# Kernel tuning notes

Measured on AMD Instinct MI355X. Metric: run time of the kernel, lower is better.

## Reference

```python
import jax, jax.numpy as jnp
import numpy as np

C, H, P = 128, 4, 8  # d_model, n_heads, n_points (n_levels=1)
D = C // H


def setup_inputs() -> dict:
    key = jax.random.key(0)
    ks = jax.random.split(key, 14)
    B, Y, X = 2, 200, 200
    N = Y * X
    s = 0.05
    inp = {
        "query": jax.random.normal(ks[0], (B, N, C), jnp.float32),
        "query_pos": jax.random.normal(ks[1], (B, N, C), jnp.float32),
        # MSDeformAttn params
        "Wv": jax.random.normal(ks[2], (C, C), jnp.float32) * s,
        "bv": jnp.zeros((C,), jnp.float32),
        "Woff": jax.random.normal(ks[3], (C, H * P * 2), jnp.float32) * s,
        "boff": jax.random.normal(ks[4], (H * P * 2,), jnp.float32) * s,
        "Wattn": jax.random.normal(ks[5], (C, H * P), jnp.float32) * s,
        "battn": jnp.zeros((H * P,), jnp.float32),
        "Wout1": jax.random.normal(ks[6], (C, C), jnp.float32) * s,  # MSDeformAttn.output_proj
        "bout1": jnp.zeros((C,), jnp.float32),
        "Wout2": jax.random.normal(ks[7], (C, C), jnp.float32) * s,  # wrapper output_proj
        "bout2": jnp.zeros((C,), jnp.float32),
        "Y": Y,
        "X": X,
    }
    return inp


def _deform_attn(q, v_in, Wv, bv, Woff, boff, Wattn, battn, Wout1, bout1, Y, X):
    B, N, _ = q.shape
    # reference points: grid centers, stacked (y, x) normalized (as in source)
    ref_y = (jnp.arange(Y, dtype=jnp.float32) + 0.5) / Y
    ref_x = (jnp.arange(X, dtype=jnp.float32) + 0.5) / X
    ry, rx = jnp.meshgrid(ref_y, ref_x, indexing="ij")
    ref = jnp.stack([ry.reshape(-1), rx.reshape(-1)], -1)  # (N, 2)

    value = (v_in @ Wv + bv).reshape(B, Y, X, H, D).transpose(0, 3, 1, 2, 4)  # (B,H,Y,X,D)
    off = (q @ Woff + boff).reshape(B, N, H, P, 2)
    attn = jax.nn.softmax((q @ Wattn + battn).reshape(B, N, H, P), axis=-1)

    # offset normalizer = (W, H) = (X, Y); loc = ref + off/norm  (faithful to source)
    norm = jnp.array([X, Y], jnp.float32)
    loc = ref[None, :, None, None, :] + off / norm  # (B,N,H,P,2)

    # grid_sample bilinear, align_corners=False, zero padding; channel 0 = x, 1 = y
    gx = loc[..., 0] * X - 0.5
    gy = loc[..., 1] * Y - 0.5
    x0 = jnp.floor(gx)
    y0 = jnp.floor(gy)
    wx1 = gx - x0
    wy1 = gy - y0
    x0i = x0.astype(jnp.int32)
    y0i = y0.astype(jnp.int32)

    b_idx = jnp.arange(B)[:, None, None, None]
    h_idx = jnp.arange(H)[None, None, :, None]

    def gather(yi, xi, w):
        valid = (yi >= 0) & (yi < Y) & (xi >= 0) & (xi < X)
        yc = jnp.clip(yi, 0, Y - 1)
        xc = jnp.clip(xi, 0, X - 1)
        v = value[b_idx, h_idx, yc, xc]  # (B,N,H,P,D)
        return v * (w * valid)[..., None]

    sampled = (
        gather(y0i, x0i, (1 - wy1) * (1 - wx1))
        + gather(y0i, x0i + 1, (1 - wy1) * wx1)
        + gather(y0i + 1, x0i, wy1 * (1 - wx1))
        + gather(y0i + 1, x0i + 1, wy1 * wx1)
    )
    out = (sampled * attn[..., None]).sum(axis=3).reshape(B, N, C)
    return out @ Wout1 + bout1


def reference(query, query_pos, Wv, bv, Woff, boff, Wattn, battn, Wout1, bout1, Wout2, bout2, Y, X):
    residual = query
    q = query + query_pos
    out = _deform_attn(q, q, Wv, bv, Woff, boff, Wattn, battn, Wout1, bout1, Y, X)
    out = out @ Wout2 + bout2  # wrapper output_proj; dropout in eval mode = identity
    return out + residual
```

## Files before the change

kernel.cpp:

```cpp
#include <hip/hip_runtime.h>
#include <hip/hip_bf16.h>

#define BQ 2
#define YY 200
#define XX 200
#define NQ 40000
#define CC 128
#define MTOT 80000
#define NCOL 224
#define NTILES 5000

typedef __attribute__((ext_vector_type(8))) short short8;
typedef __attribute__((ext_vector_type(4))) short short4v;
typedef __attribute__((ext_vector_type(4))) float f32x4;

static __device__ __forceinline__ unsigned short f2bf(float f) {
    union { float f; unsigned int u; } v; v.f = f;
    unsigned int r = v.u + 0x7FFF + ((v.u >> 16) & 1);
    return (unsigned short)(r >> 16);
}
static __device__ __forceinline__ unsigned short f2bf_hw(float f) {
    __hip_bfloat16 h = __float2bfloat16(f);
    unsigned short s;
    __builtin_memcpy(&s, &h, 2);
    return s;
}

__global__ void prep_wcat(const float* __restrict__ Wv, const float* __restrict__ Woff,
                          const float* __restrict__ Wattn, unsigned short* __restrict__ WcatT) {
    int idx = blockIdx.x * 256 + threadIdx.x;
    if (idx >= NCOL * CC) return;
    int c = idx >> 7, k = idx & 127;
    float w = (c < 128) ? Wv[k * 128 + c]
            : (c < 192) ? Woff[k * 64 + (c - 128)]
                        : Wattn[k * 32 + (c - 192)];
    WcatT[c * 128 + k] = f2bf(w);
}

__global__ void prep_w12(const float* __restrict__ Wout1, const float* __restrict__ Wout2,
                         const float* __restrict__ bout1, const float* __restrict__ bout2,
                         unsigned short* __restrict__ W12T, float* __restrict__ b12) {
    int idx = blockIdx.x * 256 + threadIdx.x;
    int c = idx >> 7, k = idx & 127;
    float s = 0.f;
    for (int j = 0; j < 128; ++j) s += Wout1[k * 128 + j] * Wout2[j * 128 + c];
    W12T[c * 128 + k] = f2bf(s);
    if (k == 0) {
        float t = bout2[c];
        for (int j = 0; j < 128; ++j) t += bout1[j] * Wout2[j * 128 + c];
        b12[c] = t;
    }
}

__global__ __launch_bounds__(256) void qsum_kernel(const float* __restrict__ query,
                                                   const float* __restrict__ qpos,
                                                   unsigned short* __restrict__ qbf) {
    const size_t total = (size_t)MTOT * CC / 8;
    for (size_t c = (size_t)blockIdx.x * 256 + threadIdx.x; c < total;
         c += (size_t)gridDim.x * 256) {
        const float4* a = (const float4*)(query + c * 8);
        const float4* b = (const float4*)(qpos + c * 8);
        float4 a0 = a[0], a1 = a[1], b0 = b[0], b1 = b[1];
        short8 w;
        w[0] = (short)f2bf_hw(a0.x + b0.x); w[1] = (short)f2bf_hw(a0.y + b0.y);
        w[2] = (short)f2bf_hw(a0.z + b0.z); w[3] = (short)f2bf_hw(a0.w + b0.w);
        w[4] = (short)f2bf_hw(a1.x + b1.x); w[5] = (short)f2bf_hw(a1.y + b1.y);
        w[6] = (short)f2bf_hw(a1.z + b1.z); w[7] = (short)f2bf_hw(a1.w + b1.w);
        *(short8*)(qbf + c * 8) = w;
    }
}

__global__ __launch_bounds__(256, 2) void g1_kernel(
    const unsigned short* __restrict__ qbf, const unsigned short* __restrict__ WcatT,
    const float* __restrict__ bv, const float* __restrict__ boff, const float* __restrict__ battn,
    unsigned short* __restrict__ value_bf, float* __restrict__ off_out, float* __restrict__ logits_out)
{
    const int tid = threadIdx.x;
    const int group = blockIdx.x & 3;
    const int gblk = blockIdx.x >> 2;
    const int lane = tid & 63;
    const int arow = lane & 15, kq = lane >> 4;
    const int wid = gblk * 4 + (tid >> 6);
    const int tg0 = group * 4;
    const int NT = (group == 3) ? 2 : 4;

    short8 bf[4][4];
#pragma unroll
    for (int t = 0; t < 4; ++t) {
        if (t < NT) {
#pragma unroll
            for (int ks = 0; ks < 4; ++ks)
                bf[t][ks] = *(const short8*)(WcatT + (size_t)((tg0 + t) * 16 + arow) * 128 + ks * 32 + kq * 8);
        }
    }

    f32x4 biasv[4];
#pragma unroll
    for (int t = 0; t < 4; ++t) {
        if (t < NT) {
            const float* bp = (group < 2) ? (bv + (tg0 + t) * 16 + kq * 4)
                            : (group == 2) ? (boff + (tg0 + t - 8) * 16 + kq * 4)
                                           : (battn + (tg0 + t - 12) * 16 + kq * 4);
            float4 b4 = *(const float4*)bp;
            biasv[t] = (f32x4){b4.x, b4.y, b4.z, b4.w};
        }
    }

    for (int tile = wid; tile < NTILES; tile += 1024) {
        const char* pa = (const char*)qbf + (size_t)(tile * 16 + arow) * 256 + kq * 16;
        short8 af[4];
#pragma unroll
        for (int ks = 0; ks < 4; ++ks) af[ks] = *(const short8*)(pa + ks * 64);

        f32x4 acc[4];
#pragma unroll
        for (int t = 0; t < 4; ++t) acc[t] = biasv[t];

#pragma unroll
        for (int ks = 0; ks < 4; ++ks) {
#pragma unroll
            for (int t = 0; t < 4; ++t) {
                if (t < NT)
                    acc[t] = __builtin_amdgcn_mfma_f32_16x16x32_bf16(bf[t][ks], af[ks], acc[t], 0, 0, 0);
            }
        }

        const int row = tile * 16 + arow;
        if (group < 2) {
#pragma unroll
            for (int t = 0; t < 4; ++t) {
                short4v pv;
                pv[0] = (short)f2bf_hw(acc[t][0]); pv[1] = (short)f2bf_hw(acc[t][1]);
                pv[2] = (short)f2bf_hw(acc[t][2]); pv[3] = (short)f2bf_hw(acc[t][3]);
                *(short4v*)(value_bf + (size_t)row * 128 + (tg0 + t) * 16 + kq * 4) = pv;
            }
        } else if (group == 2) {
#pragma unroll
            for (int t = 0; t < 4; ++t) {
                float4 o = make_float4(acc[t][0], acc[t][1], acc[t][2], acc[t][3]);
                *(float4*)(off_out + (size_t)row * 64 + (tg0 + t - 8) * 16 + kq * 4) = o;
            }
        } else {
#pragma unroll
            for (int t = 0; t < 2; ++t) {
                float4 o = make_float4(acc[t][0], acc[t][1], acc[t][2], acc[t][3]);
                *(float4*)(logits_out + (size_t)row * 32 + (tg0 + t - 12) * 16 + kq * 4) = o;
            }
        }
    }
}

__global__ __launch_bounds__(256) void sample_kernel(
    const unsigned short* __restrict__ value_bf, const float* __restrict__ off_in,
    const float* __restrict__ logits, unsigned short* __restrict__ sampled)
{
    __shared__ int S[8][32][8];

    const int tid = threadIdx.x;
    const int qi = tid >> 5;
    const int lane = tid & 31;
    const int r = blockIdx.x * 8 + qi;
    const int b = (r >= NQ) ? 1 : 0;
    const int n = r - b * NQ;
    const int yq = n / XX, xq = n - yq * XX;

    {
        float lg = logits[(size_t)r * 32 + lane];
        float m = lg;
        m = fmaxf(m, __shfl_xor(m, 1));
        m = fmaxf(m, __shfl_xor(m, 2));
        m = fmaxf(m, __shfl_xor(m, 4));
        float e = __expf(lg - m);
        float s = e;
        s += __shfl_xor(s, 1);
        s += __shfl_xor(s, 2);
        s += __shfl_xor(s, 4);
        float aw = e / s;

        float2 o = ((const float2*)(off_in + (size_t)r * 64))[lane];
        float gx = (float)yq + o.x;
        float gy = (float)xq + o.y;
        float fx = floorf(gx), fy = floorf(gy);
        int x0 = (int)fx, y0 = (int)fy;
        float wx1 = gx - fx, wy1 = gy - fy;
        float vx0 = ((unsigned)x0 < XX) ? 1.f : 0.f;
        float vx1 = ((unsigned)(x0 + 1) < XX) ? 1.f : 0.f;
        float vy0 = ((unsigned)y0 < YY) ? 1.f : 0.f;
        float vy1 = ((unsigned)(y0 + 1) < YY) ? 1.f : 0.f;
        int x0c = min(max(x0, 0), XX - 1);
        int x1c = min(max(x0 + 1, 0), XX - 1);
        int y0c = min(max(y0, 0), YY - 1);
        int y1c = min(max(y0 + 1, 0), YY - 1);
        int hb = (lane >> 3) * 64;
        int rowA = y0c * XX, rowB = y1c * XX;
        int4 addrs;
        addrs.x = (rowA + x0c) * 256 + hb;
        addrs.y = (rowA + x1c) * 256 + hb;
        addrs.z = (rowB + x0c) * 256 + hb;
        addrs.w = (rowB + x1c) * 256 + hb;
        int4 wts;
        wts.x = __float_as_int((1.f - wx1) * vx0);
        wts.y = __float_as_int(wx1 * vx1);
        wts.z = __float_as_int(aw * (1.f - wy1) * vy0);
        wts.w = __float_as_int(aw * wy1 * vy1);
        *(int4*)&S[qi][lane][0] = addrs;
        *(int4*)&S[qi][lane][4] = wts;
    }
    __syncthreads();

    const char* vb = (const char*)(value_bf + (size_t)b * NQ * 128);
    const int cb = (lane & 15) * 4;
    const int g16 = lane >> 4;

    float2 acc[2];
    acc[0] = make_float2(0.f, 0.f);
    acc[1] = make_float2(0.f, 0.f);

#pragma unroll
    for (int i = 0; i < 16; ++i) {
        const int hp = g16 * 16 + i;
        int4 ai = *(const int4*)&S[qi][hp][0];
        int4 wi = *(const int4*)&S[qi][hp][4];
        float wxa = __int_as_float(wi.x);
        float wxb = __int_as_float(wi.y);
        float wya = __int_as_float(wi.z);
        float wyb = __int_as_float(wi.w);

        unsigned int u00 = *(const unsigned int*)(vb + ai.x + cb);
        unsigned int u01 = *(const unsigned int*)(vb + ai.y + cb);
        unsigned int u10 = *(const unsigned int*)(vb + ai.z + cb);
        unsigned int u11 = *(const unsigned int*)(vb + ai.w + cb);

        float f00l = __uint_as_float(u00 << 16), f00h = __uint_as_float(u00 & 0xFFFF0000u);
        float f01l = __uint_as_float(u01 << 16), f01h = __uint_as_float(u01 & 0xFFFF0000u);
        float f10l = __uint_as_float(u10 << 16), f10h = __uint_as_float(u10 & 0xFFFF0000u);
        float f11l = __uint_as_float(u11 << 16), f11h = __uint_as_float(u11 & 0xFFFF0000u);

        float tal = fmaf(wxa, f00l, wxb * f01l);
        float tbl = fmaf(wxa, f10l, wxb * f11l);
        float tah = fmaf(wxa, f00h, wxb * f01h);
        float tbh = fmaf(wxa, f10h, wxb * f11h);

        const int j = i >> 3;
        acc[j].x = fmaf(wya, tal, acc[j].x);
        acc[j].x = fmaf(wyb, tbl, acc[j].x);
        acc[j].y = fmaf(wya, tah, acc[j].y);
        acc[j].y = fmaf(wyb, tbh, acc[j].y);
    }

    char* sp = (char*)(sampled + (size_t)r * 128);
#pragma unroll
    for (int j = 0; j < 2; ++j) {
        unsigned int packed = ((unsigned int)f2bf(acc[j].y) << 16) | (unsigned int)f2bf(acc[j].x);
        *(unsigned int*)(sp + (g16 * 2 + j) * 64 + cb) = packed;
    }
}

__global__ __launch_bounds__(256, 2) void g2_kernel(
    const unsigned short* __restrict__ sampled, const unsigned short* __restrict__ W12T,
    const float* __restrict__ b12, const float* __restrict__ query, float* __restrict__ out)
{
    const int tid = threadIdx.x;
    const int group = blockIdx.x & 1;
    const int gblk = blockIdx.x >> 1;
    const int lane = tid & 63;
    const int arow = lane & 15, kq = lane >> 4;
    const int wid = gblk * 4 + (tid >> 6);
    const int tg0 = group * 4;

    short8 bf[4][4];
#pragma unroll
    for (int t = 0; t < 4; ++t)
#pragma unroll
        for (int ks = 0; ks < 4; ++ks)
            bf[t][ks] = *(const short8*)(W12T + (size_t)((tg0 + t) * 16 + arow) * 128 + ks * 32 + kq * 8);

    f32x4 biasv[4];
#pragma unroll
    for (int t = 0; t < 4; ++t) {
        float4 b4 = *(const float4*)(b12 + (tg0 + t) * 16 + kq * 4);
        biasv[t] = (f32x4){b4.x, b4.y, b4.z, b4.w};
    }

    for (int tile = wid; tile < NTILES; tile += 2048) {
        const char* pa = (const char*)sampled + (size_t)(tile * 16 + arow) * 256 + kq * 16;
        short8 af[4];
#pragma unroll
        for (int ks = 0; ks < 4; ++ks) af[ks] = *(const short8*)(pa + ks * 64);

        f32x4 acc[4];
#pragma unroll
        for (int t = 0; t < 4; ++t) acc[t] = biasv[t];

#pragma unroll
        for (int ks = 0; ks < 4; ++ks)
#pragma unroll
            for (int t = 0; t < 4; ++t)
                acc[t] = __builtin_amdgcn_mfma_f32_16x16x32_bf16(bf[t][ks], af[ks], acc[t], 0, 0, 0);

        const int row = tile * 16 + arow;
#pragma unroll
        for (int t = 0; t < 4; ++t) {
            size_t idx = (size_t)row * 128 + (tg0 + t) * 16 + kq * 4;
            float4 q4 = *(const float4*)(query + idx);
            float4 o = make_float4(acc[t][0] + q4.x, acc[t][1] + q4.y,
                                   acc[t][2] + q4.z, acc[t][3] + q4.w);
            *(float4*)(out + idx) = o;
        }
    }
}

extern "C" void kernel_launch(void* const* d_in, const int* in_sizes, int n_in,
                              void* d_out, int out_size, void* d_ws, size_t ws_size,
                              hipStream_t stream) {
    const float* query = (const float*)d_in[0];
    const float* qpos  = (const float*)d_in[1];
    const float* Wv    = (const float*)d_in[2];
    const float* bv    = (const float*)d_in[3];
    const float* Woff  = (const float*)d_in[4];
    const float* boff  = (const float*)d_in[5];
    const float* Wattn = (const float*)d_in[6];
    const float* battn = (const float*)d_in[7];
    const float* Wout1 = (const float*)d_in[8];
    const float* bout1 = (const float*)d_in[9];
    const float* Wout2 = (const float*)d_in[10];
    const float* bout2 = (const float*)d_in[11];
    float* out = (float*)d_out;

    char* ws = (char*)d_ws;
    unsigned short* value_bf = (unsigned short*)(ws);
    float*          off_buf  = (float*)(ws + 20480000);
    float*          logits   = (float*)(ws + 40960000);
    unsigned short* sampled  = (unsigned short*)(ws + 51200000);
    unsigned short* WcatT    = (unsigned short*)(ws + 71680000);
    unsigned short* W12T     = (unsigned short*)(ws + 71680000 + 57344);
    float*          b12      = (float*)(ws + 71680000 + 57344 + 32768);

    unsigned short* qbf = sampled;

    prep_wcat<<<112, 256, 0, stream>>>(Wv, Woff, Wattn, WcatT);
    prep_w12<<<64, 256, 0, stream>>>(Wout1, Wout2, bout1, bout2, W12T, b12);
    qsum_kernel<<<2048, 256, 0, stream>>>(query, qpos, qbf);
    g1_kernel<<<1024, 256, 0, stream>>>(qbf, WcatT, bv, boff, battn,
                                        value_bf, off_buf, logits);
    sample_kernel<<<MTOT / 8, 256, 0, stream>>>(value_bf, off_buf, logits, sampled);
    g2_kernel<<<1024, 256, 0, stream>>>(sampled, W12T, b12, query, out);
}
```

Baseline: 126.2 us.

## Remap GEMM block indices, pad sample LDS tables, and use packed FMA

The GEMM kernels now map block index to column group with high bits and row block with low bits, so consecutive blocks share the same weight tile instead of interleaving groups. The sampling kernel splits its shared address/weight table into padded int4 arrays with an interleaved slot layout to cut LDS bank conflicts. It also rewrites the bilinear accumulation with 2-wide float vectors so the compiler can emit packed FMA, using split accumulators summed at the end. The remap assumes fixed grid sizes (256 and 512 row blocks per group) that must match the launch configuration.

```diff
diff --git a/kernel.cpp b/kernel.cpp
--- a/kernel.cpp
+++ b/kernel.cpp
@@ -13,6 +13,7 @@
 typedef __attribute__((ext_vector_type(8))) short short8;
 typedef __attribute__((ext_vector_type(4))) short short4v;
 typedef __attribute__((ext_vector_type(4))) float f32x4;
+typedef __attribute__((ext_vector_type(2))) float f32x2;
 
 static __device__ __forceinline__ unsigned short f2bf(float f) {
     union { float f; unsigned int u; } v; v.f = f;
@@ -76,8 +77,8 @@
     unsigned short* __restrict__ value_bf, float* __restrict__ off_out, float* __restrict__ logits_out)
 {
     const int tid = threadIdx.x;
-    const int group = blockIdx.x & 3;
-    const int gblk = blockIdx.x >> 2;
+    const int group = blockIdx.x >> 8;
+    const int gblk = blockIdx.x & 255;
     const int lane = tid & 63;
     const int arow = lane & 15, kq = lane >> 4;
     const int wid = gblk * 4 + (tid >> 6);
@@ -154,7 +155,8 @@
     const unsigned short* __restrict__ value_bf, const float* __restrict__ off_in,
     const float* __restrict__ logits, unsigned short* __restrict__ sampled)
 {
-    __shared__ int S[8][32][8];
+    __shared__ int4 SA[8][33];
+    __shared__ int4 SW[8][33];
 
     const int tid = threadIdx.x;
     const int qi = tid >> 5;
@@ -203,8 +205,9 @@
         wts.y = __float_as_int(wx1 * vx1);
         wts.z = __float_as_int(aw * (1.f - wy1) * vy0);
         wts.w = __float_as_int(aw * wy1 * vy1);
-        *(int4*)&S[qi][lane][0] = addrs;
-        *(int4*)&S[qi][lane][4] = wts;
+        const int slot = (lane & 15) * 2 + (lane >> 4);
+        SA[qi][slot] = addrs;
+        SW[qi][slot] = wts;
     }
     __syncthreads();
 
@@ -212,46 +215,43 @@
     const int cb = (lane & 15) * 4;
     const int g16 = lane >> 4;
 
-    float2 acc[2];
-    acc[0] = make_float2(0.f, 0.f);
-    acc[1] = make_float2(0.f, 0.f);
+    f32x2 acc[2][2];
+    acc[0][0] = (f32x2){0.f, 0.f}; acc[0][1] = (f32x2){0.f, 0.f};
+    acc[1][0] = (f32x2){0.f, 0.f}; acc[1][1] = (f32x2){0.f, 0.f};
 
 #pragma unroll
     for (int i = 0; i < 16; ++i) {
-        const int hp = g16 * 16 + i;
-        int4 ai = *(const int4*)&S[qi][hp][0];
-        int4 wi = *(const int4*)&S[qi][hp][4];
-        float wxa = __int_as_float(wi.x);
-        float wxb = __int_as_float(wi.y);
-        float wya = __int_as_float(wi.z);
-        float wyb = __int_as_float(wi.w);
+        const int slot = 2 * i + g16;
+        int4 ai = SA[qi][slot];
+        int4 wi = SW[qi][slot];
+        f32x2 wxa2 = (f32x2){__int_as_float(wi.x), __int_as_float(wi.x)};
+        f32x2 wxb2 = (f32x2){__int_as_float(wi.y), __int_as_float(wi.y)};
+        f32x2 wya2 = (f32x2){__int_as_float(wi.z), __int_as_float(wi.z)};
+        f32x2 wyb2 = (f32x2){__int_as_float(wi.w), __int_as_float(wi.w)};
 
         unsigned int u00 = *(const unsigned int*)(vb + ai.x + cb);
         unsigned int u01 = *(const unsigned int*)(vb + ai.y + cb);
         unsigned int u10 = *(const unsigned int*)(vb + ai.z + cb);
         unsigned int u11 = *(const unsigned int*)(vb + ai.w + cb);
 
-        float f00l = __uint_as_float(u00 << 16), f00h = __uint_as_float(u00 & 0xFFFF0000u);
-        float f01l = __uint_as_float(u01 << 16), f01h = __uint_as_float(u01 & 0xFFFF0000u);
-        float f10l = __uint_as_float(u10 << 16), f10h = __uint_as_float(u10 & 0xFFFF0000u);
-        float f11l = __uint_as_float(u11 << 16), f11h = __uint_as_float(u11 & 0xFFFF0000u);
-
-        float tal = fmaf(wxa, f00l, wxb * f01l);
-        float tbl = fmaf(wxa, f10l, wxb * f11l);
-        float tah = fmaf(wxa, f00h, wxb * f01h);
-        float tbh = fmaf(wxa, f10h, wxb * f11h);
-
-        const int j = i >> 3;
-        acc[j].x = fmaf(wya, tal, acc[j].x);
-        acc[j].x = fmaf(wyb, tbl, acc[j].x);
-        acc[j].y = fmaf(wya, tah, acc[j].y);
-        acc[j].y = fmaf(wyb, tbh, acc[j].y);
+        f32x2 f00 = (f32x2){__uint_as_float(u00 << 16), __uint_as_float(u00 & 0xFFFF0000u)};
+        f32x2 f01 = (f32x2){__uint_as_float(u01 << 16), __uint_as_float(u01 & 0xFFFF0000u)};
+        f32x2 f10 = (f32x2){__uint_as_float(u10 << 16), __uint_as_float(u10 & 0xFFFF0000u)};
+        f32x2 f11 = (f32x2){__uint_as_float(u11 << 16), __uint_as_float(u11 & 0xFFFF0000u)};
+
+        f32x2 ta = __builtin_elementwise_fma(wxa2, f00, wxb2 * f01);
+        f32x2 tb = __builtin_elementwise_fma(wxa2, f10, wxb2 * f11);
+
+        const int j = i >> 3, k = i & 1;
+        acc[j][k] = __builtin_elementwise_fma(wya2, ta, acc[j][k]);
+        acc[j][k] = __builtin_elementwise_fma(wyb2, tb, acc[j][k]);
     }
 
     char* sp = (char*)(sampled + (size_t)r * 128);
 #pragma unroll
     for (int j = 0; j < 2; ++j) {
-        unsigned int packed = ((unsigned int)f2bf(acc[j].y) << 16) | (unsigned int)f2bf(acc[j].x);
+        f32x2 a2 = acc[j][0] + acc[j][1];
+        unsigned int packed = ((unsigned int)f2bf(a2[1]) << 16) | (unsigned int)f2bf(a2[0]);
         *(unsigned int*)(sp + (g16 * 2 + j) * 64 + cb) = packed;
     }
 }
@@ -261,8 +261,8 @@
     const float* __restrict__ b12, const float* __restrict__ query, float* __restrict__ out)
 {
     const int tid = threadIdx.x;
-    const int group = blockIdx.x & 1;
-    const int gblk = blockIdx.x >> 1;
+    const int group = blockIdx.x >> 9;
+    const int gblk = blockIdx.x & 511;
     const int lane = tid & 63;
     const int arow = lane & 15, kq = lane >> 4;
     const int wid = gblk * 4 + (tid >> 6);
```

Result: faster. 121.0 us (-4.2%).
